# Optimization experiments

Hardware: AMD Instinct MI355X
Metric: run time of the kernel (lower is better)

The kernel has to match this reference:

```python
import jax, jax.numpy as jnp
import numpy as np

N, M = 131072, 12
ORIG, NBR, AF, H, NP, NCONV, N0 = 92, 41, 64, 128, 2, 3, 1024
EPS = 1e-5


def _bn(x, gamma, beta):
    # training-mode BatchNorm1d: biased batch stats over axis 0
    mean = jnp.mean(x, axis=0)
    var = jnp.mean((x - mean) ** 2, axis=0)
    return gamma * (x - mean) * jax.lax.rsqrt(var + EPS) + beta


def setup_inputs() -> dict:
    key = jax.random.key(0)
    ks = jax.random.split(key, 16)
    atom_fea = jax.random.normal(ks[0], (N, ORIG), dtype=jnp.float32)
    nbr_fea = jax.random.normal(ks[1], (N, M, NBR), dtype=jnp.float32)
    nbr_fea_idx = jax.random.randint(ks[2], (N, M), 0, N)
    crystal_atom_idx = jnp.sort(jax.random.randint(ks[3], (N,), 0, N0))
    FIN = 2 * AF + NBR  # 169
    W_embed = jax.random.normal(ks[4], (ORIG, AF), dtype=jnp.float32) / np.sqrt(ORIG)
    b_embed = jnp.zeros((AF,), jnp.float32)
    conv_W = jax.random.normal(ks[5], (NCONV, FIN, 2 * AF), dtype=jnp.float32) / np.sqrt(FIN)
    conv_b = jnp.zeros((NCONV, 2 * AF), jnp.float32)
    conv_g1 = jnp.ones((NCONV, 2 * AF), jnp.float32)
    conv_be1 = jnp.zeros((NCONV, 2 * AF), jnp.float32)
    conv_g2 = jnp.ones((NCONV, AF), jnp.float32)
    conv_be2 = jnp.zeros((NCONV, AF), jnp.float32)
    head_W1 = jax.random.normal(ks[6], (NP, AF, H), dtype=jnp.float32) / np.sqrt(AF)
    head_b1 = jnp.zeros((NP, H), jnp.float32)
    head_W2 = jax.random.normal(ks[7], (NP, H, 1), dtype=jnp.float32) / np.sqrt(H)
    head_b2 = jnp.zeros((NP, 1), jnp.float32)
    return dict(atom_fea=atom_fea, nbr_fea=nbr_fea,
                W_embed=W_embed, b_embed=b_embed,
                conv_W=conv_W, conv_b=conv_b,
                conv_g1=conv_g1, conv_be1=conv_be1,
                conv_g2=conv_g2, conv_be2=conv_be2,
                head_W1=head_W1, head_b1=head_b1,
                head_W2=head_W2, head_b2=head_b2,
                nbr_fea_idx=nbr_fea_idx, crystal_atom_idx=crystal_atom_idx)


def reference(atom_fea, nbr_fea, W_embed, b_embed, conv_W, conv_b,
              conv_g1, conv_be1, conv_g2, conv_be2,
              head_W1, head_b1, head_W2, head_b2,
              nbr_fea_idx, crystal_atom_idx):
    x = atom_fea @ W_embed + b_embed  # (N, AF)
    for l in range(NCONV):
        nbr = x[nbr_fea_idx]                                   # (N, M, AF) gather
        self_f = jnp.broadcast_to(x[:, None, :], (N, M, AF))
        tot = jnp.concatenate([self_f, nbr, nbr_fea], axis=2)  # (N, M, 2AF+NBR)
        gated = tot @ conv_W[l] + conv_b[l]                    # (N, M, 2AF)
        gated = _bn(gated.reshape(-1, 2 * AF), conv_g1[l], conv_be1[l]).reshape(N, M, 2 * AF)
        nbr_filter = jax.nn.sigmoid(gated[..., :AF])
        nbr_core = jax.nn.softplus(gated[..., AF:])
        nbr_sumed = jnp.sum(nbr_filter * nbr_core, axis=1)     # (N, AF)
        nbr_sumed = _bn(nbr_sumed, conv_g2[l], conv_be2[l])
        x = jax.nn.softplus(x + nbr_sumed)
    # per-crystal mean pooling
    sums = jax.ops.segment_sum(x, crystal_atom_idx, num_segments=N0)
    counts = jax.ops.segment_sum(jnp.ones((N,), x.dtype), crystal_atom_idx, num_segments=N0)
    crys_fea = sums / jnp.maximum(counts, 1.0)[:, None]        # (N0, AF)
    a = jax.nn.softplus(crys_fea)
    h = jax.nn.softplus(jnp.einsum('nf,pfh->pnh', a, head_W1) + head_b1[:, None, :])
    out = jnp.einsum('pnh,pho->pno', h, head_W2) + head_b2[:, None, :]  # (P, N0, 1)
    out = jnp.transpose(out[..., 0])                           # (N0, P)
    return out, crys_fea
```

## Files before the change

### kernel.cpp

```cpp
#include <hip/hip_runtime.h>

#define N_ATOMS 131072
#define M_NBR 12
#define ORIG_F 92
#define AF 64
#define NCONV 3
#define N0_CRYS 1024
#define FIN 169
#define C2 128
#define KPAD 192
#define BN_EPS 1e-5f
#define RB_TOTAL (N_ATOMS * M_NBR / 64)
#define BT_TOTAL (N_ATOMS * M_NBR / 96)

typedef _Float16 f16;
typedef _Float16 half8 __attribute__((ext_vector_type(8)));
typedef float f32x4 __attribute__((ext_vector_type(4)));

union H8 { half8 h; ushort4 u[2]; };

__device__ __forceinline__ float fexp_(float t) {
    float r; asm("v_exp_f32 %0, %1" : "=v"(r) : "v"(t * 1.44269504f)); return r;
}
__device__ __forceinline__ float flog_(float t) {
    float r; asm("v_log_f32 %0, %1" : "=v"(r) : "v"(t)); return r * 0.69314718f;
}
__device__ __forceinline__ float frcp_(float t) {
    float r; asm("v_rcp_f32 %0, %1" : "=v"(r) : "v"(t)); return r;
}
__device__ __forceinline__ float sigmoidf_(float t) {
    return frcp_(1.0f + fexp_(-t));
}
__device__ __forceinline__ float softplusf_(float t) {
    return fmaxf(t, 0.0f) + flog_(1.0f + fexp_(-fabsf(t)));
}

__global__ __launch_bounds__(256) void k_embed(const float* __restrict__ af,
                                               const float* __restrict__ W,
                                               const float* __restrict__ b,
                                               float* __restrict__ x,
                                               f16* __restrict__ xh) {
    __shared__ float Wl[ORIG_F * AF];
    const int tid = threadIdx.x;
    for (int i = tid; i < ORIG_F * AF / 4; i += 256)
        *(f32x4*)&Wl[i * 4] = *(const f32x4*)&W[i * 4];
    __syncthreads();

    const int a = tid >> 4;
    const int f0 = (tid & 15) * 4;
    const f32x4 bias = *(const f32x4*)&b[f0];

#pragma unroll
    for (int ch = 0; ch < 8; ++ch) {
        const int n = blockIdx.x * 128 + ch * 16 + a;
        const float* ar = af + (size_t)n * ORIG_F;
        f32x4 acc = bias;
        for (int k4 = 0; k4 < 23; ++k4) {
            f32x4 av = *(const f32x4*)&ar[k4 * 4];
#pragma unroll
            for (int e = 0; e < 4; ++e) {
                f32x4 wv = *(const f32x4*)&Wl[(k4 * 4 + e) * AF + f0];
#pragma unroll
                for (int j = 0; j < 4; ++j)
                    acc[j] = fmaf(av[e], wv[j], acc[j]);
            }
        }
        *(f32x4*)&x[(size_t)n * AF + f0] = acc;
        f16 h4[4] = {(f16)acc[0], (f16)acc[1], (f16)acc[2], (f16)acc[3]};
        *(ushort4*)&xh[(size_t)n * AF + f0] = *(const ushort4*)h4;
    }
}

__global__ __launch_bounds__(256) void k_cvt_nbrf(const float* __restrict__ nf,
                                                  f16* __restrict__ nfh) {
    const int r0 = blockIdx.x * 32;
    for (int i = threadIdx.x; i < 32 * 22; i += 256) {
        int r = i / 22, k2 = i - r * 22;
        size_t row = (size_t)(r0 + r);
        int k = k2 * 2;
        float f0 = (k < 41) ? nf[row * 41 + k] : 0.0f;
        float f1 = (k + 1 < 41) ? nf[row * 41 + k + 1] : 0.0f;
        f16 two[2] = {(f16)f0, (f16)f1};
        *(ushort2*)&nfh[row * 44 + k] = *(const ushort2*)two;
    }
}

__global__ __launch_bounds__(256) void k_prepW(const float* __restrict__ W,
                                               f16* __restrict__ Wt) {
    int i = blockIdx.x * 256 + threadIdx.x;
    if (i >= C2 * KPAD) return;
    int c = i / KPAD, k = i - c * KPAD;
    Wt[i] = (k < FIN) ? (f16)W[k * C2 + c] : (f16)0.0f;
}

__global__ __launch_bounds__(256) void k_gemmA(const f16* __restrict__ xh,
                                               const f16* __restrict__ nfh,
                                               const int* __restrict__ nidx,
                                               const f16* __restrict__ Wt,
                                               const float* __restrict__ bl,
                                               float* __restrict__ stats) {
    __shared__ float redS[128], redQ[128];

    const int tid = threadIdx.x;
    const int wv = tid >> 6;
    const int lane = tid & 63;
    const int quad = lane >> 4;
    const int l16 = lane & 15;
    const int rhalf = wv >> 1;
    const int c0w = (wv & 1) * 64;
    const unsigned q16 = (unsigned)quad * 16u;

    if (tid < 128) { redS[tid] = 0.0f; redQ[tid] = 0.0f; }

    half8 Bf[6][4];
    float bias_[4];
    float ssum[4] = {0, 0, 0, 0}, ssq[4] = {0, 0, 0, 0};
    int niter = 0;
#pragma unroll
    for (int ct = 0; ct < 4; ++ct) {
        int c = c0w + ct * 16 + l16;
        bias_[ct] = bl[c];
#pragma unroll
        for (int kc = 0; kc < 6; ++kc)
            Bf[kc][ct] = *(const half8*)&Wt[c * KPAD + kc * 32 + quad * 8];
    }

    const char* xb = (const char*)xh;
    const char* nb = (const char*)nfh;
    const ushort4 z4 = make_ushort4(0, 0, 0, 0);

    int ng0 = 0, ng1 = 0;
    {
        const int row0 = blockIdx.x * 64 + rhalf * 32 + l16;
        ng0 = nidx[row0];
        ng1 = nidx[row0 + 16];
    }

    for (int rb = blockIdx.x; rb < RB_TOTAL; rb += gridDim.x) {
        const int rbn = rb + gridDim.x;
        int ng0n = 0, ng1n = 0;
        if (rbn < RB_TOTAL) {
            const int rown = rbn * 64 + rhalf * 32 + l16;
            ng0n = nidx[rown];
            ng1n = nidx[rown + 16];
        }

        const int row0 = rb * 64 + rhalf * 32 + l16;
        const int row1 = row0 + 16;
        const unsigned os0 = (unsigned)((unsigned)row0 / 12u) * 128u + q16;
        const unsigned os1 = (unsigned)((unsigned)row1 / 12u) * 128u + q16;
        const unsigned og0 = (unsigned)ng0 * 128u + q16;
        const unsigned og1 = (unsigned)ng1 * 128u + q16;
        const unsigned on0 = (unsigned)row0 * 88u;
        const unsigned on1 = (unsigned)row1 * 88u;

        H8 a0[6], a1[6];
        a0[0].h = *(const half8*)(xb + os0);
        a0[1].h = *(const half8*)(xb + os0 + 64u);
        a0[2].h = *(const half8*)(xb + og0);
        a0[3].h = *(const half8*)(xb + og0 + 64u);
        a0[4].u[0] = *(const ushort4*)(nb + on0 + q16);
        a0[4].u[1] = *(const ushort4*)(nb + on0 + q16 + 8u);
        a0[5].u[0] = z4; a0[5].u[1] = z4;
        if (quad == 0) {
            a0[5].u[0] = *(const ushort4*)(nb + on0 + 64u);
            a0[5].u[1] = *(const ushort4*)(nb + on0 + 72u);
        } else if (quad == 1) {
            a0[5].u[0] = *(const ushort4*)(nb + on0 + 80u);
        }
        a1[0].h = *(const half8*)(xb + os1);
        a1[1].h = *(const half8*)(xb + os1 + 64u);
        a1[2].h = *(const half8*)(xb + og1);
        a1[3].h = *(const half8*)(xb + og1 + 64u);
        a1[4].u[0] = *(const ushort4*)(nb + on1 + q16);
        a1[4].u[1] = *(const ushort4*)(nb + on1 + q16 + 8u);
        a1[5].u[0] = z4; a1[5].u[1] = z4;
        if (quad == 0) {
            a1[5].u[0] = *(const ushort4*)(nb + on1 + 64u);
            a1[5].u[1] = *(const ushort4*)(nb + on1 + 72u);
        } else if (quad == 1) {
            a1[5].u[0] = *(const ushort4*)(nb + on1 + 80u);
        }

        f32x4 acc[2][4];
#pragma unroll
        for (int rf = 0; rf < 2; ++rf)
#pragma unroll
            for (int ct = 0; ct < 4; ++ct) acc[rf][ct] = (f32x4){0, 0, 0, 0};

#pragma unroll
        for (int kc = 0; kc < 6; ++kc) {
#pragma unroll
            for (int ct = 0; ct < 4; ++ct) {
                acc[0][ct] = __builtin_amdgcn_mfma_f32_16x16x32_f16(a0[kc].h, Bf[kc][ct], acc[0][ct], 0, 0, 0);
                acc[1][ct] = __builtin_amdgcn_mfma_f32_16x16x32_f16(a1[kc].h, Bf[kc][ct], acc[1][ct], 0, 0, 0);
            }
        }

#pragma unroll
        for (int rf = 0; rf < 2; ++rf)
#pragma unroll
            for (int ct = 0; ct < 4; ++ct)
#pragma unroll
                for (int e = 0; e < 4; ++e) {
                    float v = acc[rf][ct][e];
                    ssum[ct] += v;
                    ssq[ct] = fmaf(v, v, ssq[ct]);
                }
        ++niter;
        ng0 = ng0n; ng1 = ng1n;
    }

    const float cnt = 8.0f * (float)niter;
#pragma unroll
    for (int ct = 0; ct < 4; ++ct) {
        float b = bias_[ct];
        float S = ssum[ct];
        ssq[ct] = ssq[ct] + 2.0f * b * S + cnt * b * b;
        ssum[ct] = S + cnt * b;
    }

    __syncthreads();
#pragma unroll
    for (int ct = 0; ct < 4; ++ct) {
        float s = ssum[ct], q = ssq[ct];
        s += __shfl_xor(s, 16); s += __shfl_xor(s, 32);
        q += __shfl_xor(q, 16); q += __shfl_xor(q, 32);
        if (quad == 0) {
            atomicAdd(&redS[c0w + ct * 16 + l16], s);
            atomicAdd(&redQ[c0w + ct * 16 + l16], q);
        }
    }
    __syncthreads();
    if (tid < 128) {
        atomicAdd(&stats[tid], redS[tid]);
        atomicAdd(&stats[128 + tid], redQ[tid]);
    }
}

__global__ __launch_bounds__(256) void k_gemmB(const f16* __restrict__ xh,
                                               const f16* __restrict__ nfh,
                                               const int* __restrict__ nidx,
                                               const f16* __restrict__ Wt,
                                               const float* __restrict__ bl,
                                               const float* __restrict__ g1,
                                               const float* __restrict__ be1,
                                               float* __restrict__ stats,
                                               float* __restrict__ ns) {
    __shared__ float scr[4][12][33];
    __shared__ float rs[64], rq[64];

    const int tid = threadIdx.x;
    const int wv = tid >> 6;
    const int lane = tid & 63;
    const int quad = lane >> 4;
    const int l16 = lane & 15;
    const int rgrp = wv >> 1;
    const int csel = wv & 1;
    const unsigned q16 = (unsigned)quad * 16u;
    const float cnt1 = (float)N_ATOMS * M_NBR;

    if (tid < 64) { rs[tid] = 0.0f; rq[tid] = 0.0f; }
    __syncthreads();

    const int tmap[4] = {2 * csel, 2 * csel + 1, 4 + 2 * csel, 5 + 2 * csel};
    float P[4], Q[4];
    half8 Bf[4][6];
#pragma unroll
    for (int jt = 0; jt < 4; ++jt) {
        int c = tmap[jt] * 16 + l16;
        float m1 = stats[c] / cnt1;
        float v1 = stats[128 + c] / cnt1 - m1 * m1;
        float A1 = g1[c] * rsqrtf(v1 + BN_EPS);
        P[jt] = A1;
        Q[jt] = fmaf(A1, bl[c], be1[c] - A1 * m1);
#pragma unroll
        for (int kc = 0; kc < 6; ++kc)
            Bf[jt][kc] = *(const half8*)&Wt[c * KPAD + kc * 32 + quad * 8];
    }

    const char* xb = (const char*)xh;
    const char* nb = (const char*)nfh;
    const ushort4 z4 = make_ushort4(0, 0, 0, 0);
    float ls[2] = {0, 0}, lq2[2] = {0, 0};

    int ng[3];
    {
        const int rw = blockIdx.x * 96 + rgrp * 48;
#pragma unroll
        for (int rt = 0; rt < 3; ++rt) ng[rt] = nidx[rw + rt * 16 + l16];
    }

    for (int bt = blockIdx.x; bt < BT_TOTAL; bt += gridDim.x) {
        const int btn = bt + gridDim.x;
        int ngn[3] = {0, 0, 0};
        if (btn < BT_TOTAL) {
            const int rwn = btn * 96 + rgrp * 48;
#pragma unroll
            for (int rt = 0; rt < 3; ++rt) ngn[rt] = nidx[rwn + rt * 16 + l16];
        }

        const int rw = bt * 96 + rgrp * 48;
        float part[3][2];
#pragma unroll
        for (int rt = 0; rt < 3; ++rt) {
            const int r = rw + rt * 16 + l16;
            const unsigned osf = (unsigned)((unsigned)r / 12u) * 128u + q16;
            const unsigned ogf = (unsigned)ng[rt] * 128u + q16;
            const unsigned onf = (unsigned)r * 88u;
            H8 a[6];
            a[0].h = *(const half8*)(xb + osf);
            a[1].h = *(const half8*)(xb + osf + 64u);
            a[2].h = *(const half8*)(xb + ogf);
            a[3].h = *(const half8*)(xb + ogf + 64u);
            a[4].u[0] = *(const ushort4*)(nb + onf + q16);
            a[4].u[1] = *(const ushort4*)(nb + onf + q16 + 8u);
            a[5].u[0] = z4; a[5].u[1] = z4;
            if (quad == 0) {
                a[5].u[0] = *(const ushort4*)(nb + onf + 64u);
                a[5].u[1] = *(const ushort4*)(nb + onf + 72u);
            } else if (quad == 1) {
                a[5].u[0] = *(const ushort4*)(nb + onf + 80u);
            }

            f32x4 acc[4];
#pragma unroll
            for (int jt = 0; jt < 4; ++jt) acc[jt] = (f32x4){0, 0, 0, 0};
#pragma unroll
            for (int kc = 0; kc < 6; ++kc)
#pragma unroll
                for (int jt = 0; jt < 4; ++jt)
                    acc[jt] = __builtin_amdgcn_mfma_f32_16x16x32_f16(a[kc].h, Bf[jt][kc], acc[jt], 0, 0, 0);

#pragma unroll
            for (int j = 0; j < 2; ++j) {
                float s = 0.0f;
#pragma unroll
                for (int e = 0; e < 4; ++e) {
                    float vf = fmaf(P[j],     acc[j][e],     Q[j]);
                    float vc = fmaf(P[j + 2], acc[j + 2][e], Q[j + 2]);
                    s = fmaf(sigmoidf_(vf), softplusf_(vc), s);
                }
                part[rt][j] = s;
            }
        }
#pragma unroll
        for (int rt = 0; rt < 3; ++rt)
#pragma unroll
            for (int j = 0; j < 2; ++j)
                scr[wv][rt * 4 + quad][j * 16 + l16] = part[rt][j];
#pragma unroll
        for (int j = 0; j < 2; ++j) {
            int cj = j * 16 + l16;
            float s = scr[wv][3 * quad][cj] + scr[wv][3 * quad + 1][cj] + scr[wv][3 * quad + 2][cj];
            const int n = bt * 8 + rgrp * 4 + quad;
            ns[(size_t)n * 64 + csel * 32 + cj] = s;
            ls[j] += s;
            lq2[j] = fmaf(s, s, lq2[j]);
        }
        ng[0] = ngn[0]; ng[1] = ngn[1]; ng[2] = ngn[2];
    }

#pragma unroll
    for (int j = 0; j < 2; ++j) {
        float s = ls[j], q = lq2[j];
        s += __shfl_xor(s, 16); s += __shfl_xor(s, 32);
        q += __shfl_xor(q, 16); q += __shfl_xor(q, 32);
        if (quad == 0) {
            atomicAdd(&rs[csel * 32 + j * 16 + l16], s);
            atomicAdd(&rq[csel * 32 + j * 16 + l16], q);
        }
    }
    __syncthreads();
    if (tid < 64) {
        atomicAdd(&stats[256 + tid], rs[tid]);
        atomicAdd(&stats[320 + tid], rq[tid]);
    }
}

__global__ __launch_bounds__(256) void k_convC2(float* __restrict__ x,
                                                f16* __restrict__ xh,
                                                const float* __restrict__ ns,
                                                const float* __restrict__ g2,
                                                const float* __restrict__ be2,
                                                const float* __restrict__ stats,
                                                const float* __restrict__ Wn,
                                                f16* __restrict__ Wt,
                                                int do_prep) {
    const int tid = threadIdx.x;
    if (blockIdx.x < 8192) {
        const int i4 = blockIdx.x * 256 + tid;
        const size_t base = (size_t)i4 * 4;
        const int f0 = (int)(base & 63);
        const float cnt = (float)N_ATOMS;
        f32x4 m4 = *(const f32x4*)&stats[256 + f0];
        f32x4 q4 = *(const f32x4*)&stats[320 + f0];
        f32x4 g4 = *(const f32x4*)&g2[f0];
        f32x4 b4 = *(const f32x4*)&be2[f0];
        f32x4 xv = *(const f32x4*)&x[base];
        f32x4 nv = *(const f32x4*)&ns[base];
        f16 h4[4];
#pragma unroll
        for (int j = 0; j < 4; ++j) {
            float m = m4[j] / cnt;
            float v = q4[j] / cnt - m * m;
            float A = g4[j] * rsqrtf(v + BN_EPS);
            float B = b4[j] - A * m;
            float o = softplusf_(xv[j] + fmaf(A, nv[j], B));
            xv[j] = o;
            h4[j] = (f16)o;
        }
        *(f32x4*)&x[base] = xv;
        *(ushort4*)&xh[base] = *(const ushort4*)h4;
    } else if (do_prep) {
        const int i = (blockIdx.x - 8192) * 256 + tid;
        if (i < C2 * KPAD) {
            int c = i / KPAD, k = i - c * KPAD;
            Wt[i] = (k < FIN) ? (f16)Wn[k * C2 + c] : (f16)0.0f;
        }
    }
}

__global__ __launch_bounds__(64) void k_pool(const float* __restrict__ x,
                                             const int* __restrict__ cidx,
                                             float* __restrict__ crys) {
    const int s = blockIdx.x;
    const int f = threadIdx.x;
    int lo = 0, hi = N_ATOMS;
    while (lo < hi) { int mid = (lo + hi) >> 1; if (cidx[mid] < s) lo = mid + 1; else hi = mid; }
    int lo2 = lo, hi2 = N_ATOMS;
    while (lo2 < hi2) { int mid = (lo2 + hi2) >> 1; if (cidx[mid] < s + 1) lo2 = mid + 1; else hi2 = mid; }
    float sum = 0.0f;
    for (int i = lo; i < lo2; ++i) sum += x[(size_t)i * 64 + f];
    float cnt = fmaxf((float)(lo2 - lo), 1.0f);
    crys[s * 64 + f] = sum / cnt;
}

__global__ __launch_bounds__(128) void k_head(const float* __restrict__ crys,
                                              const float* __restrict__ W1,
                                              const float* __restrict__ b1,
                                              const float* __restrict__ W2,
                                              const float* __restrict__ b2,
                                              float* __restrict__ out) {
    __shared__ float a_sh[64];
    __shared__ float r_sh[128];
    const int n = blockIdx.x;
    const int tid = threadIdx.x;
    if (tid < 64) a_sh[tid] = softplusf_(crys[n * 64 + tid]);
    __syncthreads();
    for (int p = 0; p < 2; ++p) {
        float acc = b1[p * 128 + tid];
#pragma unroll
        for (int f2 = 0; f2 < 64; ++f2)
            acc = fmaf(a_sh[f2], W1[(p * 64 + f2) * 128 + tid], acc);
        float contrib = softplusf_(acc) * W2[p * 128 + tid];
        r_sh[tid] = contrib;
        __syncthreads();
        for (int sft = 64; sft > 0; sft >>= 1) {
            if (tid < sft) r_sh[tid] += r_sh[tid + sft];
            __syncthreads();
        }
        if (tid == 0) out[n * 2 + p] = r_sh[0] + b2[p];
        __syncthreads();
    }
}

extern "C" void kernel_launch(void* const* d_in, const int* in_sizes, int n_in,
                              void* d_out, int out_size, void* d_ws, size_t ws_size,
                              hipStream_t stream) {
    const float* atom_fea = (const float*)d_in[0];
    const float* nbr_fea  = (const float*)d_in[1];
    const float* W_embed  = (const float*)d_in[2];
    const float* b_embed  = (const float*)d_in[3];
    const float* conv_W   = (const float*)d_in[4];
    const float* conv_b   = (const float*)d_in[5];
    const float* conv_g1  = (const float*)d_in[6];
    const float* conv_be1 = (const float*)d_in[7];
    const float* conv_g2  = (const float*)d_in[8];
    const float* conv_be2 = (const float*)d_in[9];
    const float* head_W1  = (const float*)d_in[10];
    const float* head_b1  = (const float*)d_in[11];
    const float* head_W2  = (const float*)d_in[12];
    const float* head_b2  = (const float*)d_in[13];
    const int*   nidx     = (const int*)d_in[14];
    const int*   cryst    = (const int*)d_in[15];

    char* w = (char*)d_ws;
    float* x      = (float*)w;
    f16*   xh     = (f16*)(w + 33554432);
    float* ns     = (float*)(w + 50331648);
    f16*   nfh    = (f16*)(w + 83886080);
    f16*   Wt     = (f16*)(w + 222298112);
    float* stats  = (float*)(w + 222347264);
    const size_t required = 222347264ull + 4608ull;
    if (ws_size < required) {
        hipMemsetAsync(d_out, 0x7F, 4, stream);
        return;
    }

    hipMemsetAsync(stats, 0, NCONV * 384 * sizeof(float), stream);

    k_cvt_nbrf<<<N_ATOMS * M_NBR / 32, 256, 0, stream>>>(nbr_fea, nfh);
    k_embed<<<N_ATOMS / 128, 256, 0, stream>>>(atom_fea, W_embed, b_embed, x, xh);
    k_prepW<<<(C2 * KPAD + 255) / 256, 256, 0, stream>>>(conv_W, Wt);

    for (int l = 0; l < NCONV; ++l) {
        float* st = stats + l * 384;
        k_gemmA<<<2048, 256, 0, stream>>>(xh, nfh, nidx, Wt, conv_b + l * C2, st);
        k_gemmB<<<2048, 256, 0, stream>>>(xh, nfh, nidx, Wt, conv_b + l * C2,
                                          conv_g1 + l * C2, conv_be1 + l * C2, st, ns);
        const int ln = (l + 1 < NCONV) ? l + 1 : l;
        k_convC2<<<8288, 256, 0, stream>>>(x, xh, ns, conv_g2 + l * AF, conv_be2 + l * AF, st,
                                           conv_W + (size_t)ln * FIN * C2, Wt, (l + 1 < NCONV) ? 1 : 0);
    }

    float* crys = (float*)d_out + N0_CRYS * 2;
    k_pool<<<N0_CRYS, 64, 0, stream>>>(x, cryst, crys);
    k_head<<<N0_CRYS, 128, 0, stream>>>(crys, head_W1, head_b1, head_W2, head_b2, (float*)d_out);
}
```

Baseline: 1.376 ms.

## Precompute per-atom self and neighbor projections before the BN-stats pass

```diff
diff --git a/kernel.cpp b/kernel.cpp
--- a/kernel.cpp
+++ b/kernel.cpp
@@ -93,14 +93,10 @@
     Wt[i] = (k < FIN) ? (f16)W[k * C2 + c] : (f16)0.0f;
 }
 
-__global__ __launch_bounds__(256) void k_gemmA(const f16* __restrict__ xh,
-                                               const f16* __restrict__ nfh,
-                                               const int* __restrict__ nidx,
-                                               const f16* __restrict__ Wt,
-                                               const float* __restrict__ bl,
-                                               float* __restrict__ stats) {
-    __shared__ float redS[128], redQ[128];
-
+__global__ __launch_bounds__(256) void k_zy(const f16* __restrict__ xh,
+                                            const f16* __restrict__ Wt,
+                                            float* __restrict__ z,
+                                            float* __restrict__ y) {
     const int tid = threadIdx.x;
     const int wv = tid >> 6;
     const int lane = tid & 63;
@@ -110,76 +106,130 @@
     const int c0w = (wv & 1) * 64;
     const unsigned q16 = (unsigned)quad * 16u;
 
-    if (tid < 128) { redS[tid] = 0.0f; redQ[tid] = 0.0f; }
-
-    half8 Bf[6][4];
-    float bias_[4];
-    float ssum[4] = {0, 0, 0, 0}, ssq[4] = {0, 0, 0, 0};
-    int niter = 0;
+    half8 Bz[4][2], By[4][2];
 #pragma unroll
     for (int ct = 0; ct < 4; ++ct) {
         int c = c0w + ct * 16 + l16;
-        bias_[ct] = bl[c];
-#pragma unroll
-        for (int kc = 0; kc < 6; ++kc)
-            Bf[kc][ct] = *(const half8*)&Wt[c * KPAD + kc * 32 + quad * 8];
-    }
-
+        Bz[ct][0] = *(const half8*)&Wt[c * KPAD + quad * 8];
+        Bz[ct][1] = *(const half8*)&Wt[c * KPAD + 32 + quad * 8];
+        By[ct][0] = *(const half8*)&Wt[c * KPAD + 64 + quad * 8];
+        By[ct][1] = *(const half8*)&Wt[c * KPAD + 96 + quad * 8];
+    }
     const char* xb = (const char*)xh;
+    const unsigned na0 = (unsigned)(blockIdx.x * 64 + rhalf * 32 + l16);
+    const unsigned na1 = na0 + 16u;
+    half8 a0[2], a1[2];
+    a0[0] = *(const half8*)(xb + na0 * 128u + q16);
+    a0[1] = *(const half8*)(xb + na0 * 128u + 64u + q16);
+    a1[0] = *(const half8*)(xb + na1 * 128u + q16);
+    a1[1] = *(const half8*)(xb + na1 * 128u + 64u + q16);
+
+    f32x4 az[2][4], ay[2][4];
+#pragma unroll
+    for (int rf = 0; rf < 2; ++rf)
+#pragma unroll
+        for (int ct = 0; ct < 4; ++ct) { az[rf][ct] = (f32x4){0, 0, 0, 0}; ay[rf][ct] = (f32x4){0, 0, 0, 0}; }
+#pragma unroll
+    for (int kc = 0; kc < 2; ++kc)
+#pragma unroll
+        for (int ct = 0; ct < 4; ++ct) {
+            az[0][ct] = __builtin_amdgcn_mfma_f32_16x16x32_f16(a0[kc], Bz[ct][kc], az[0][ct], 0, 0, 0);
+            az[1][ct] = __builtin_amdgcn_mfma_f32_16x16x32_f16(a1[kc], Bz[ct][kc], az[1][ct], 0, 0, 0);
+            ay[0][ct] = __builtin_amdgcn_mfma_f32_16x16x32_f16(a0[kc], By[ct][kc], ay[0][ct], 0, 0, 0);
+            ay[1][ct] = __builtin_amdgcn_mfma_f32_16x16x32_f16(a1[kc], By[ct][kc], ay[1][ct], 0, 0, 0);
+        }
+
+#pragma unroll
+    for (int rf = 0; rf < 2; ++rf) {
+        int rbase = blockIdx.x * 64 + rhalf * 32 + rf * 16 + quad * 4;
+#pragma unroll
+        for (int ct = 0; ct < 4; ++ct) {
+            int c = c0w + ct * 16 + l16;
+#pragma unroll
+            for (int e = 0; e < 4; ++e) {
+                z[(size_t)(rbase + e) * 128 + c] = az[rf][ct][e];
+                y[(size_t)(rbase + e) * 128 + c] = ay[rf][ct][e];
+            }
+        }
+    }
+}
+
+__global__ __launch_bounds__(256) void k_gemmA(const f16* __restrict__ nfh,
+                                               const int* __restrict__ nidx,
+                                               const f16* __restrict__ Wt,
+                                               const float* __restrict__ z,
+                                               const float* __restrict__ y,
+                                               const float* __restrict__ bl,
+                                               float* __restrict__ stats) {
+    __shared__ float redS[128], redQ[128];
+    const int tid = threadIdx.x;
+    const int wv = tid >> 6;
+    const int lane = tid & 63;
+    const int quad = lane >> 4;
+    const int l16 = lane & 15;
+    const int rhalf = wv >> 1;
+    const int c0w = (wv & 1) * 64;
+    const unsigned q16 = (unsigned)quad * 16u;
+    const int q4 = quad * 4;
+
+    if (tid < 128) { redS[tid] = 0.0f; redQ[tid] = 0.0f; }
+
+    half8 Bf[4][2];
+#pragma unroll
+    for (int ct = 0; ct < 4; ++ct) {
+        int c = c0w + ct * 16 + l16;
+        Bf[ct][0] = *(const half8*)&Wt[c * KPAD + 128 + quad * 8];
+        Bf[ct][1] = *(const half8*)&Wt[c * KPAD + 160 + quad * 8];
+    }
+
+    f32x4 ssum[4], ssq[4];
+#pragma unroll
+    for (int ct = 0; ct < 4; ++ct) { ssum[ct] = (f32x4){0, 0, 0, 0}; ssq[ct] = (f32x4){0, 0, 0, 0}; }
+    int niter = 0;
     const char* nb = (const char*)nfh;
     const ushort4 z4 = make_ushort4(0, 0, 0, 0);
 
     int ng0 = 0, ng1 = 0;
     {
-        const int row0 = blockIdx.x * 64 + rhalf * 32 + l16;
-        ng0 = nidx[row0];
-        ng1 = nidx[row0 + 16];
+        const int r0 = blockIdx.x * 64 + rhalf * 32 + l16;
+        ng0 = nidx[r0];
+        ng1 = nidx[r0 + 16];
     }
 
     for (int rb = blockIdx.x; rb < RB_TOTAL; rb += gridDim.x) {
         const int rbn = rb + gridDim.x;
         int ng0n = 0, ng1n = 0;
         if (rbn < RB_TOTAL) {
-            const int rown = rbn * 64 + rhalf * 32 + l16;
-            ng0n = nidx[rown];
-            ng1n = nidx[rown + 16];
-        }
-
-        const int row0 = rb * 64 + rhalf * 32 + l16;
-        const int row1 = row0 + 16;
-        const unsigned os0 = (unsigned)((unsigned)row0 / 12u) * 128u + q16;
-        const unsigned os1 = (unsigned)((unsigned)row1 / 12u) * 128u + q16;
-        const unsigned og0 = (unsigned)ng0 * 128u + q16;
-        const unsigned og1 = (unsigned)ng1 * 128u + q16;
-        const unsigned on0 = (unsigned)row0 * 88u;
-        const unsigned on1 = (unsigned)row1 * 88u;
-
-        H8 a0[6], a1[6];
-        a0[0].h = *(const half8*)(xb + os0);
-        a0[1].h = *(const half8*)(xb + os0 + 64u);
-        a0[2].h = *(const half8*)(xb + og0);
-        a0[3].h = *(const half8*)(xb + og0 + 64u);
-        a0[4].u[0] = *(const ushort4*)(nb + on0 + q16);
-        a0[4].u[1] = *(const ushort4*)(nb + on0 + q16 + 8u);
-        a0[5].u[0] = z4; a0[5].u[1] = z4;
+            const int rn = rbn * 64 + rhalf * 32 + l16;
+            ng0n = nidx[rn];
+            ng1n = nidx[rn + 16];
+        }
+
+        const int r0 = rb * 64 + rhalf * 32 + l16;
+        const int r1 = r0 + 16;
+        const unsigned n0 = (unsigned)r0 / 12u;
+        const unsigned n1 = (unsigned)r1 / 12u;
+        const unsigned on0 = (unsigned)r0 * 88u;
+        const unsigned on1 = (unsigned)r1 * 88u;
+
+        H8 a0[2], a1[2];
+        a0[0].u[0] = *(const ushort4*)(nb + on0 + q16);
+        a0[0].u[1] = *(const ushort4*)(nb + on0 + q16 + 8u);
+        a0[1].u[0] = z4; a0[1].u[1] = z4;
         if (quad == 0) {
-            a0[5].u[0] = *(const ushort4*)(nb + on0 + 64u);
-            a0[5].u[1] = *(const ushort4*)(nb + on0 + 72u);
+            a0[1].u[0] = *(const ushort4*)(nb + on0 + 64u);
+            a0[1].u[1] = *(const ushort4*)(nb + on0 + 72u);
         } else if (quad == 1) {
-            a0[5].u[0] = *(const ushort4*)(nb + on0 + 80u);
-        }
-        a1[0].h = *(const half8*)(xb + os1);
-        a1[1].h = *(const half8*)(xb + os1 + 64u);
-        a1[2].h = *(const half8*)(xb + og1);
-        a1[3].h = *(const half8*)(xb + og1 + 64u);
-        a1[4].u[0] = *(const ushort4*)(nb + on1 + q16);
-        a1[4].u[1] = *(const ushort4*)(nb + on1 + q16 + 8u);
-        a1[5].u[0] = z4; a1[5].u[1] = z4;
+            a0[1].u[0] = *(const ushort4*)(nb + on0 + 80u);
+        }
+        a1[0].u[0] = *(const ushort4*)(nb + on1 + q16);
+        a1[0].u[1] = *(const ushort4*)(nb + on1 + q16 + 8u);
+        a1[1].u[0] = z4; a1[1].u[1] = z4;
         if (quad == 0) {
-            a1[5].u[0] = *(const ushort4*)(nb + on1 + 64u);
-            a1[5].u[1] = *(const ushort4*)(nb + on1 + 72u);
+            a1[1].u[0] = *(const ushort4*)(nb + on1 + 64u);
+            a1[1].u[1] = *(const ushort4*)(nb + on1 + 72u);
         } else if (quad == 1) {
-            a1[5].u[0] = *(const ushort4*)(nb + on1 + 80u);
+            a1[1].u[0] = *(const ushort4*)(nb + on1 + 80u);
         }
 
         f32x4 acc[2][4];
@@ -189,52 +239,61 @@
             for (int ct = 0; ct < 4; ++ct) acc[rf][ct] = (f32x4){0, 0, 0, 0};
 
 #pragma unroll
-        for (int kc = 0; kc < 6; ++kc) {
+        for (int kc = 0; kc < 2; ++kc)
 #pragma unroll
             for (int ct = 0; ct < 4; ++ct) {
-                acc[0][ct] = __builtin_amdgcn_mfma_f32_16x16x32_f16(a0[kc].h, Bf[kc][ct], acc[0][ct], 0, 0, 0);
-                acc[1][ct] = __builtin_amdgcn_mfma_f32_16x16x32_f16(a1[kc].h, Bf[kc][ct], acc[1][ct], 0, 0, 0);
-            }
-        }
-
-#pragma unroll
-        for (int rf = 0; rf < 2; ++rf)
-#pragma unroll
-            for (int ct = 0; ct < 4; ++ct)
-#pragma unroll
-                for (int e = 0; e < 4; ++e) {
-                    float v = acc[rf][ct][e];
-                    ssum[ct] += v;
-                    ssq[ct] = fmaf(v, v, ssq[ct]);
-                }
+                acc[0][ct] = __builtin_amdgcn_mfma_f32_16x16x32_f16(Bf[ct][kc], a0[kc].h, acc[0][ct], 0, 0, 0);
+                acc[1][ct] = __builtin_amdgcn_mfma_f32_16x16x32_f16(Bf[ct][kc], a1[kc].h, acc[1][ct], 0, 0, 0);
+            }
+
+#pragma unroll
+        for (int ct = 0; ct < 4; ++ct) {
+            const int cb = c0w + ct * 16 + q4;
+            f32x4 zv0 = *(const f32x4*)&z[(size_t)n0 * 128 + cb];
+            f32x4 yv0 = *(const f32x4*)&y[(size_t)ng0 * 128 + cb];
+            f32x4 zv1 = *(const f32x4*)&z[(size_t)n1 * 128 + cb];
+            f32x4 yv1 = *(const f32x4*)&y[(size_t)ng1 * 128 + cb];
+#pragma unroll
+            for (int e = 0; e < 4; ++e) {
+                float v0 = acc[0][ct][e] + zv0[e] + yv0[e];
+                float v1 = acc[1][ct][e] + zv1[e] + yv1[e];
+                ssum[ct][e] += v0 + v1;
+                ssq[ct][e] = fmaf(v0, v0, fmaf(v1, v1, ssq[ct][e]));
+            }
+        }
         ++niter;
         ng0 = ng0n; ng1 = ng1n;
     }
 
-    const float cnt = 8.0f * (float)niter;
-#pragma unroll
-    for (int ct = 0; ct < 4; ++ct) {
-        float b = bias_[ct];
-        float S = ssum[ct];
-        ssq[ct] = ssq[ct] + 2.0f * b * S + cnt * b * b;
-        ssum[ct] = S + cnt * b;
-    }
-
+#pragma unroll
+    for (int ct = 0; ct < 4; ++ct)
+#pragma unroll
+        for (int e = 0; e < 4; ++e) {
+            float s = ssum[ct][e], q = ssq[ct][e];
+            s += __shfl_xor(s, 1); s += __shfl_xor(s, 2);
+            s += __shfl_xor(s, 4); s += __shfl_xor(s, 8);
+            q += __shfl_xor(q, 1); q += __shfl_xor(q, 2);
+            q += __shfl_xor(q, 4); q += __shfl_xor(q, 8);
+            ssum[ct][e] = s; ssq[ct][e] = q;
+        }
     __syncthreads();
-#pragma unroll
-    for (int ct = 0; ct < 4; ++ct) {
-        float s = ssum[ct], q = ssq[ct];
-        s += __shfl_xor(s, 16); s += __shfl_xor(s, 32);
-        q += __shfl_xor(q, 16); q += __shfl_xor(q, 32);
-        if (quad == 0) {
-            atomicAdd(&redS[c0w + ct * 16 + l16], s);
-            atomicAdd(&redQ[c0w + ct * 16 + l16], q);
-        }
+    if (l16 == 0) {
+#pragma unroll
+        for (int ct = 0; ct < 4; ++ct)
+#pragma unroll
+            for (int e = 0; e < 4; ++e) {
+                int c = c0w + ct * 16 + q4 + e;
+                atomicAdd(&redS[c], ssum[ct][e]);
+                atomicAdd(&redQ[c], ssq[ct][e]);
+            }
     }
     __syncthreads();
     if (tid < 128) {
-        atomicAdd(&stats[tid], redS[tid]);
-        atomicAdd(&stats[128 + tid], redQ[tid]);
+        float b = bl[tid];
+        float S = redS[tid];
+        float cntB = 64.0f * (float)niter;
+        atomicAdd(&stats[tid], fmaf(cntB, b, S));
+        atomicAdd(&stats[128 + tid], redQ[tid] + 2.0f * b * S + cntB * b * b);
     }
 }
 
@@ -492,7 +551,9 @@
     f16*   nfh    = (f16*)(w + 83886080);
     f16*   Wt     = (f16*)(w + 222298112);
     float* stats  = (float*)(w + 222347264);
-    const size_t required = 222347264ull + 4608ull;
+    float* z      = (float*)(w + 222351872);
+    float* y      = (float*)(w + 289460736);
+    const size_t required = 356569600ull;
     if (ws_size < required) {
         hipMemsetAsync(d_out, 0x7F, 4, stream);
         return;
@@ -506,7 +567,8 @@
 
     for (int l = 0; l < NCONV; ++l) {
         float* st = stats + l * 384;
-        k_gemmA<<<2048, 256, 0, stream>>>(xh, nfh, nidx, Wt, conv_b + l * C2, st);
+        k_zy<<<N_ATOMS / 64, 256, 0, stream>>>(xh, Wt, z, y);
+        k_gemmA<<<2048, 256, 0, stream>>>(nfh, nidx, Wt, z, y, conv_b + l * C2, st);
         k_gemmB<<<2048, 256, 0, stream>>>(xh, nfh, nidx, Wt, conv_b + l * C2,
                                           conv_g1 + l * C2, conv_be1 + l * C2, st, ns);
         const int ln = (l + 1 < NCONV) ? l + 1 : l;
```

New measurement: 1.651 ms. +20.0%, slower.
